# Performance work log

Hardware: AMD Instinct MI355X
Metric: run time of the kernel (lower is better)

Reference implementation:

```python
import jax, jax.numpy as jnp
import numpy as np

B, S, D, H = 2, 2048, 1024, 16
DH = D // H  # 64


def setup_inputs() -> dict:
    key = jax.random.key(0)
    k1, k2, k3 = jax.random.split(key, 3)
    return {
        "x": jax.random.normal(k1, (B, S, D), dtype=jnp.float32),
        "w_qkv": jax.random.normal(k2, (D, 3 * D), dtype=jnp.float32) * 0.02,
        "b_qkv": jnp.zeros((3 * D,), dtype=jnp.float32),
        "w_out": jax.random.normal(k3, (D, D), dtype=jnp.float32) * 0.02,
        "b_out": jnp.zeros((D,), dtype=jnp.float32),
    }


def reference(x, w_qkv, b_qkv, w_out, b_out):
    # fused qkv projection: [B,S,3D]
    qkv = x @ w_qkv + b_qkv
    q, k, v = qkv[..., :D], qkv[..., D:2 * D], qkv[..., 2 * D:]
    # split heads -> [B,H,S,DH]
    split = lambda t: t.reshape(B, S, H, DH).transpose(0, 2, 1, 3)
    q, k, v = split(q), split(k), split(v)
    scale = 1.0 / jnp.sqrt(jnp.asarray(DH, dtype=x.dtype))
    scores = jnp.einsum("bhqd,bhkd->bhqk", q, k) * scale  # [B,H,S,S]
    attn = jax.nn.softmax(scores, axis=-1)
    out = jnp.einsum("bhqk,bhkd->bhqd", attn, v)  # [B,H,S,DH]
    out = out.transpose(0, 2, 1, 3).reshape(B, S, D)
    return out @ w_out + b_out
```

## Files before the change

kernel.cpp:

```cpp
#include <hip/hip_runtime.h>
#include <cstdint>

#define B_ 2
#define S_ 2048
#define D_ 1024
#define H_ 16
#define DH_ 64

typedef short bf16x8 __attribute__((ext_vector_type(8)));
typedef float f32x4 __attribute__((ext_vector_type(4)));

__device__ inline unsigned short f2bf(float f) {
  unsigned int u = __float_as_uint(f);
  u += 0x7fffu + ((u >> 16) & 1u);
  return (unsigned short)(u >> 16);
}

__device__ inline float bf2f(unsigned short h) {
  return __uint_as_float(((unsigned int)h) << 16);
}

__device__ inline float fexp2(float x) { return __builtin_amdgcn_exp2f(x); }

__device__ inline int swz(int row, int bytecol) {
  return row * 128 + (bytecol ^ ((row & 7) << 4));
}

#define GLL(gp, lp)                                                            \
  __builtin_amdgcn_global_load_lds(                                            \
      (const __attribute__((address_space(1))) unsigned int*)(gp),             \
      (__attribute__((address_space(3))) unsigned int*)(lp), 16, 0, 0)

__global__ __launch_bounds__(256) void k_prep(const float* __restrict__ x,
                                              unsigned short* __restrict__ xb,
                                              const float* __restrict__ w_qkv,
                                              unsigned short* __restrict__ wqT,
                                              const float* __restrict__ w_out,
                                              unsigned short* __restrict__ woT) {
  __shared__ float tile[32][33];
  const int bid = blockIdx.x;
  const int t = threadIdx.x;
  if (bid < 4096) {
    int i = bid * 256 + t;
    float4 v = reinterpret_cast<const float4*>(x)[i];
    ushort4 o;
    o.x = f2bf(v.x); o.y = f2bf(v.y); o.z = f2bf(v.z); o.w = f2bf(v.w);
    reinterpret_cast<ushort4*>(xb)[i] = o;
    return;
  }
  const float* in;
  unsigned short* out;
  int R, C, bx, by;
  if (bid < 7168) {
    int id = bid - 4096;
    bx = id % 96; by = id / 96;
    in = w_qkv; out = wqT; R = 1024; C = 3072;
  } else {
    int id = bid - 7168;
    bx = id & 31; by = id >> 5;
    in = w_out; out = woT; R = 1024; C = 1024;
  }
  int ct = bx * 32, rt = by * 32;
  int tx = t & 31, ty = t >> 5;
#pragma unroll
  for (int i = 0; i < 32; i += 8)
    tile[ty + i][tx] = in[(size_t)(rt + ty + i) * C + ct + tx];
  __syncthreads();
#pragma unroll
  for (int i = 0; i < 32; i += 8)
    out[(size_t)(ct + ty + i) * R + rt + tx] = f2bf(tile[tx][ty + i]);
}

template <int BM, int BN, typename OutT>
__global__ __launch_bounds__(256) void k_gemm(const unsigned short* __restrict__ A,
                                              const unsigned short* __restrict__ BT,
                                              const float* __restrict__ bias,
                                              OutT* __restrict__ C,
                                              unsigned short* __restrict__ VTout,
                                              int M, int N, int K) {
  constexpr int MT = BM / 32, NT = BN / 32;
  __shared__ unsigned short As[BM * 64];
  __shared__ unsigned short Bs[BN * 64];
  const int t = threadIdx.x;
  const int lane = t & 63;
  const int wave = t >> 6;
  const int wm = wave >> 1, wn = wave & 1;
  const int ln15 = lane & 15, lg = lane >> 4;
  const int nwg = gridDim.x * gridDim.y;
  const int flat = blockIdx.y * gridDim.x + blockIdx.x;
  const int cpx = nwg >> 3;
  const int sid = (flat & 7) * cpx + (flat >> 3);
  const int row0 = (sid % gridDim.x) * BM, col0 = (sid / gridDim.x) * BN;
  f32x4 acc[MT][NT];
#pragma unroll
  for (int i = 0; i < MT; ++i)
#pragma unroll
    for (int j = 0; j < NT; ++j)
      acc[i][j] = (f32x4){0.f, 0.f, 0.f, 0.f};

  for (int k0 = 0; k0 < K; k0 += 64) {
    __syncthreads();
#pragma unroll
    for (int i = 0; i < BM / 32; ++i) {
      int chunk = i * 256 + t;
      int r = chunk >> 3;
      int cb = (chunk & 7) * 16;
      GLL((const char*)(A + (size_t)(row0 + r) * K + k0) + cb, (char*)As + chunk * 16);
    }
#pragma unroll
    for (int i = 0; i < BN / 32; ++i) {
      int chunk = i * 256 + t;
      int r = chunk >> 3;
      int cb = (chunk & 7) * 16;
      GLL((const char*)(BT + (size_t)(col0 + r) * K + k0) + cb, (char*)Bs + chunk * 16);
    }
    __syncthreads();
#pragma unroll
    for (int ks = 0; ks < 2; ++ks) {
      bf16x8 af[MT], bf[NT];
#pragma unroll
      for (int mt = 0; mt < MT; ++mt)
        af[mt] = *(const bf16x8*)&As[(wm * (BM / 2) + mt * 16 + ln15) * 64 + ks * 32 + lg * 8];
#pragma unroll
      for (int nt = 0; nt < NT; ++nt)
        bf[nt] = *(const bf16x8*)&Bs[(wn * (BN / 2) + nt * 16 + ln15) * 64 + ks * 32 + lg * 8];
#pragma unroll
      for (int mt = 0; mt < MT; ++mt)
#pragma unroll
        for (int nt = 0; nt < NT; ++nt)
          acc[mt][nt] = __builtin_amdgcn_mfma_f32_16x16x32_bf16(af[mt], bf[nt], acc[mt][nt], 0, 0, 0);
    }
  }
#pragma unroll
  for (int mt = 0; mt < MT; ++mt) {
#pragma unroll
    for (int nt = 0; nt < NT; ++nt) {
      int col = col0 + wn * (BN / 2) + nt * 16 + ln15;
      float bv = bias[col];
      if (VTout != nullptr && col >= 2048) {
        int hd = col - 2048;
        int row = row0 + wm * (BM / 2) + mt * 16 + lg * 4;
        int bb = row >> 11, ss = row & 2047;
        ushort4 o;
        o.x = f2bf(acc[mt][nt][0] + bv);
        o.y = f2bf(acc[mt][nt][1] + bv);
        o.z = f2bf(acc[mt][nt][2] + bv);
        o.w = f2bf(acc[mt][nt][3] + bv);
        *(ushort4*)&VTout[(((size_t)(bb * 16 + (hd >> 6)) * 64) + (hd & 63)) * 2048 + ss] = o;
      } else {
#pragma unroll
        for (int r = 0; r < 4; ++r) {
          int row = row0 + wm * (BM / 2) + mt * 16 + lg * 4 + r;
          float v = acc[mt][nt][r] + bv;
          if constexpr (sizeof(OutT) == 2)
            C[(size_t)row * N + col] = f2bf(v);
          else
            C[(size_t)row * N + col] = v;
        }
      }
    }
  }
}

__global__ __launch_bounds__(512) void k_attn(const unsigned short* __restrict__ qkv,
                                              const unsigned short* __restrict__ VT,
                                              unsigned short* __restrict__ O) {
  __shared__ unsigned short Ks[2][64 * 64];
  __shared__ unsigned short Vs[2][64 * 64];
  __shared__ unsigned short Ps[8][16 * 64];

  const int bid = blockIdx.x;
  const int xcd = bid & 7, idx = bid >> 3;
  const int bh = xcd + (idx >> 4) * 8;
  const int qblk = idx & 15;
  const int b = bh >> 4, h = bh & 15;
  const int t = threadIdx.x, wave = t >> 6, lane = t & 63;
  const int ln15 = lane & 15, lg = lane >> 4;
  const unsigned short* Qb = qkv + (size_t)b * S_ * 3072 + h * 64;
  const unsigned short* Kb = Qb + 1024;
  const unsigned short* Vb = VT + (size_t)bh * 64 * 2048;
  const int q0 = qblk * 128 + wave * 16;

  const float qsc = 0.125f * 1.4426950408889634f;
  bf16x8 qf[2];
#pragma unroll
  for (int ks = 0; ks < 2; ++ks) {
    bf16x8 raw = *(const bf16x8*)&Qb[(size_t)(q0 + ln15) * 3072 + ks * 32 + lg * 8];
#pragma unroll
    for (int j = 0; j < 8; ++j)
      qf[ks][j] = (short)f2bf(bf2f((unsigned short)raw[j]) * qsc);
  }

  const int srow = t >> 3;
  const int scol = (t & 7) ^ (srow & 7);
  const unsigned short* kPtr0 = Kb + (size_t)srow * 3072 + scol * 8;
  const unsigned short* vPtr0 = Vb + (size_t)srow * 2048 + scol * 8;
  char* ldsK0 = (char*)&Ks[0][0] + t * 16;
  char* ldsV0 = (char*)&Vs[0][0] + t * 16;

  auto stage = [&](int bi, int kv) {
    GLL(kPtr0 + (size_t)kv * 3072, ldsK0 + bi * 8192);
    GLL(vPtr0 + kv, ldsV0 + bi * 8192);
  };

  f32x4 acc[4];
#pragma unroll
  for (int dt = 0; dt < 4; ++dt)
    acc[dt] = (f32x4){0.f, 0.f, 0.f, 0.f};
  float m0 = -1e30f, l0 = 0.f;
  unsigned short* Pw = Ps[wave];

  stage(0, 0);
  __syncthreads();
  int buf = 0;

  for (int kv = 0; kv < S_; kv += 64) {
    if (kv + 64 < S_) stage(buf ^ 1, kv + 64);

    f32x4 st[4];
#pragma unroll
    for (int kg = 0; kg < 4; ++kg)
      st[kg] = (f32x4){0.f, 0.f, 0.f, 0.f};
    __builtin_amdgcn_s_setprio(1);
#pragma unroll
    for (int kg = 0; kg < 4; ++kg) {
      int krow = kg * 16 + ln15;
      bf16x8 kf0 = *(const bf16x8*)((const char*)&Ks[buf][0] + swz(krow, lg * 16));
      bf16x8 kf1 = *(const bf16x8*)((const char*)&Ks[buf][0] + swz(krow, 64 + lg * 16));
      st[kg] = __builtin_amdgcn_mfma_f32_16x16x32_bf16(kf0, qf[0], st[kg], 0, 0, 0);
      st[kg] = __builtin_amdgcn_mfma_f32_16x16x32_bf16(kf1, qf[1], st[kg], 0, 0, 0);
    }
    __builtin_amdgcn_s_setprio(0);

    float tm = -1e30f;
#pragma unroll
    for (int kg = 0; kg < 4; ++kg)
      tm = fmaxf(tm, fmaxf(fmaxf(st[kg][0], st[kg][1]),
                           fmaxf(st[kg][2], st[kg][3])));
    tm = fmaxf(tm, __shfl_xor(tm, 16));
    tm = fmaxf(tm, __shfl_xor(tm, 32));

    if (__any(tm > m0 + 11.0f)) {
      float n0 = fmaxf(m0, tm);
      float r0 = fexp2(m0 - n0);
      m0 = n0; l0 *= r0;
#pragma unroll
      for (int dt = 0; dt < 4; ++dt)
#pragma unroll
        for (int r = 0; r < 4; ++r)
          acc[dt][r] *= r0;
    }

    asm volatile("" ::: "memory");
    float ts = 0.f;
#pragma unroll
    for (int kg = 0; kg < 4; ++kg) {
      float p0 = fexp2(st[kg][0] - m0);
      float p1 = fexp2(st[kg][1] - m0);
      float p2 = fexp2(st[kg][2] - m0);
      float p3 = fexp2(st[kg][3] - m0);
      ts += (p0 + p1) + (p2 + p3);
      unsigned int w0, w1;
      asm("v_cvt_pk_bf16_f32 %0, %1, %2" : "=v"(w0) : "v"(p0), "v"(p1));
      asm("v_cvt_pk_bf16_f32 %0, %1, %2" : "=v"(w1) : "v"(p2), "v"(p3));
      *(uint2*)((char*)Pw + swz(ln15, kg * 32 + lg * 8)) = make_uint2(w0, w1);
    }
    ts += __shfl_xor(ts, 16);
    ts += __shfl_xor(ts, 32);
    l0 += ts;
    asm volatile("" ::: "memory");

    __builtin_amdgcn_s_setprio(1);
#pragma unroll
    for (int kc = 0; kc < 2; ++kc) {
      bf16x8 pf = *(const bf16x8*)((const char*)Pw + swz(ln15, kc * 64 + lg * 16));
#pragma unroll
      for (int dt = 0; dt < 4; ++dt) {
        bf16x8 vf = *(const bf16x8*)((const char*)&Vs[buf][0] + swz(dt * 16 + ln15, kc * 64 + lg * 16));
        acc[dt] = __builtin_amdgcn_mfma_f32_16x16x32_bf16(vf, pf, acc[dt], 0, 0, 0);
      }
    }
    __builtin_amdgcn_s_setprio(0);
    __syncthreads();
    buf ^= 1;
  }

  float inv = 1.f / l0;
  size_t qglob = q0 + ln15;
  size_t base = ((size_t)b * S_ + qglob) * D_ + h * 64 + lg * 4;
#pragma unroll
  for (int dt = 0; dt < 4; ++dt) {
    ushort4 o;
    o.x = f2bf(acc[dt][0] * inv);
    o.y = f2bf(acc[dt][1] * inv);
    o.z = f2bf(acc[dt][2] * inv);
    o.w = f2bf(acc[dt][3] * inv);
    *(ushort4*)&O[base + (size_t)dt * 16] = o;
  }
}

extern "C" void kernel_launch(void* const* d_in, const int* in_sizes, int n_in,
                              void* d_out, int out_size, void* d_ws, size_t ws_size,
                              hipStream_t stream) {
  const float* x     = (const float*)d_in[0];
  const float* w_qkv = (const float*)d_in[1];
  const float* b_qkv = (const float*)d_in[2];
  const float* w_out = (const float*)d_in[3];
  const float* b_out = (const float*)d_in[4];
  float* out = (float*)d_out;

  char* ws = (char*)d_ws;
  const size_t MiB = (size_t)1 << 20;
  unsigned short* xb   = (unsigned short*)(ws + 0 * MiB);
  unsigned short* wqT  = (unsigned short*)(ws + 8 * MiB);
  unsigned short* woT  = (unsigned short*)(ws + 14 * MiB);
  unsigned short* qkvb = (unsigned short*)(ws + 16 * MiB);
  unsigned short* VTb  = (unsigned short*)(ws + 40 * MiB);
  unsigned short* Ab   = (unsigned short*)(ws + 48 * MiB);

  k_prep<<<8192, 256, 0, stream>>>(x, xb, w_qkv, wqT, w_out, woT);
  k_gemm<128, 128, unsigned short><<<dim3(32, 24), 256, 0, stream>>>(xb, wqT, b_qkv, qkvb, VTb, 4096, 3072, 1024);
  k_attn<<<512, 512, 0, stream>>>(qkvb, VTb, Ab);
  k_gemm<128, 64, float><<<dim3(32, 16), 256, 0, stream>>>(Ab, woT, b_out, out, nullptr, 4096, 1024, 1024);
}
```

Measured before the change: 217.1 us.

## Replace QKV GEMM with 256x256 double-buffered 8-wave pipelined kernel

Adds a new GEMM kernel with 256x256 tiles, 512 threads, double-buffered swizzled LDS, and global loads staged in four pieces interleaved with MFMA quarters, using partial vmcnt waits and setprio. It replaces the QKV projection GEMM, which now runs on 192 workgroups instead of 768. The intent is to overlap global-to-LDS transfers with compute and get more operand reuse per tile. The risks are low grid occupancy on a 256-CU device (192 blocks), heavy register pressure, and fragile hand-written waitcnt logic. The V-transpose epilogue is removed from the old kernel, which now only serves the output GEMM.

```diff
diff --git a/kernel.cpp b/kernel.cpp
--- a/kernel.cpp
+++ b/kernel.cpp
@@ -71,6 +71,163 @@
     out[(size_t)(ct + ty + i) * R + rt + tx] = f2bf(tile[tx][ty + i]);
 }
 
+#define READB(p)                                                               \
+  _Pragma("unroll") for (int nt = 0; nt < 4; ++nt)                             \
+  _Pragma("unroll") for (int ks = 0; ks < 2; ++ks)                             \
+      bf[nt][ks] = *(const bf16x8*)((const char*)&Bs[cur][0] +                 \
+                   swz((p) * 64 + nt * 16 + ln15, ks * 64 + lg * 16));
+
+#define STAGEPIECE(h)                                                          \
+  _Pragma("unroll") for (int j = 0; j < 2; ++j) {                              \
+    const int rr = ((h) & 1) * 128 + srow + 64 * j;                            \
+    const int gc = scol8 ^ (rr & 7);                                           \
+    const unsigned short* gsrc =                                               \
+        (((h) < 2) ? (A + (size_t)(row0 + rr) * K)                             \
+                   : (BT + (size_t)(col0 + rr) * K)) + k0n + gc * 8;           \
+    char* ldst = (char*)(((h) < 2) ? &As[cur ^ 1][0] : &Bs[cur ^ 1][0]) +      \
+                 rr * 128 + scol8 * 16;                                        \
+    GLL(gsrc, ldst);                                                           \
+  }
+
+#define MFMAQ(p)                                                               \
+  _Pragma("unroll") for (int mt = 0; mt < 2; ++mt)                             \
+  _Pragma("unroll") for (int nt = 0; nt < 4; ++nt) {                           \
+    acc[mt][(p) * 4 + nt] = __builtin_amdgcn_mfma_f32_16x16x32_bf16(           \
+        af[mt][0], bf[nt][0], acc[mt][(p) * 4 + nt], 0, 0, 0);                 \
+    acc[mt][(p) * 4 + nt] = __builtin_amdgcn_mfma_f32_16x16x32_bf16(           \
+        af[mt][1], bf[nt][1], acc[mt][(p) * 4 + nt], 0, 0, 0);                 \
+  }
+
+template <typename OutT>
+__global__ __launch_bounds__(512, 2) void k_gemm8(const unsigned short* __restrict__ A,
+                                                  const unsigned short* __restrict__ BT,
+                                                  const float* __restrict__ bias,
+                                                  OutT* __restrict__ C,
+                                                  unsigned short* __restrict__ VTout,
+                                                  int M, int N, int K) {
+  __shared__ unsigned short As[2][256 * 64];
+  __shared__ unsigned short Bs[2][256 * 64];
+  const int t = threadIdx.x;
+  const int lane = t & 63;
+  const int w = t >> 6;
+  const int ln15 = lane & 15, lg = lane >> 4;
+  const int srow = t >> 3;
+  const int scol8 = t & 7;
+  const int nwg = gridDim.x * gridDim.y;
+  const int flat = blockIdx.y * gridDim.x + blockIdx.x;
+  const int cpx = nwg >> 3;
+  const int sid = (flat & 7) * cpx + (flat >> 3);
+  const int row0 = (sid % gridDim.x) * 256, col0 = (sid / gridDim.x) * 256;
+
+  f32x4 acc[2][16];
+#pragma unroll
+  for (int i = 0; i < 2; ++i)
+#pragma unroll
+    for (int j = 0; j < 16; ++j)
+      acc[i][j] = (f32x4){0.f, 0.f, 0.f, 0.f};
+
+  const int NTILES = K / 64;
+  {
+    const int k0n = 0;
+    const int cur = 1;
+    STAGEPIECE(0); STAGEPIECE(1); STAGEPIECE(2); STAGEPIECE(3);
+  }
+  asm volatile("s_waitcnt vmcnt(0)" ::: "memory");
+  __builtin_amdgcn_s_barrier();
+
+  int cur = 0;
+  for (int kt = 0; kt < NTILES; ++kt) {
+    const int k0n = (kt + 1) * 64;
+    const bool more = (kt + 1) < NTILES;
+    bf16x8 af[2][2];
+    {
+      bf16x8 bf[4][2];
+      READB(0);
+#pragma unroll
+      for (int mt = 0; mt < 2; ++mt)
+#pragma unroll
+        for (int ks = 0; ks < 2; ++ks)
+          af[mt][ks] = *(const bf16x8*)((const char*)&As[cur][0] +
+                       swz(w * 32 + mt * 16 + ln15, ks * 64 + lg * 16));
+      if (more) { STAGEPIECE(0); }
+      __builtin_amdgcn_s_barrier();
+      __builtin_amdgcn_s_setprio(1);
+      MFMAQ(0);
+      __builtin_amdgcn_s_setprio(0);
+      __builtin_amdgcn_s_barrier();
+    }
+    {
+      bf16x8 bf[4][2];
+      READB(1);
+      if (more) {
+        STAGEPIECE(1);
+        asm volatile("s_waitcnt vmcnt(4)" ::: "memory");
+      } else {
+        asm volatile("s_waitcnt vmcnt(0)" ::: "memory");
+      }
+      __builtin_amdgcn_s_barrier();
+      __builtin_amdgcn_s_setprio(1);
+      MFMAQ(1);
+      __builtin_amdgcn_s_setprio(0);
+      __builtin_amdgcn_s_barrier();
+    }
+    {
+      bf16x8 bf[4][2];
+      READB(2);
+      if (more) { STAGEPIECE(2); }
+      __builtin_amdgcn_s_barrier();
+      __builtin_amdgcn_s_setprio(1);
+      MFMAQ(2);
+      __builtin_amdgcn_s_setprio(0);
+      __builtin_amdgcn_s_barrier();
+    }
+    {
+      bf16x8 bf[4][2];
+      READB(3);
+      if (more) {
+        STAGEPIECE(3);
+        asm volatile("s_waitcnt vmcnt(2)" ::: "memory");
+      }
+      __builtin_amdgcn_s_barrier();
+      __builtin_amdgcn_s_setprio(1);
+      MFMAQ(3);
+      __builtin_amdgcn_s_setprio(0);
+      __builtin_amdgcn_s_barrier();
+    }
+    cur ^= 1;
+  }
+
+#pragma unroll
+  for (int mt = 0; mt < 2; ++mt) {
+#pragma unroll
+    for (int nt = 0; nt < 16; ++nt) {
+      int col = col0 + nt * 16 + ln15;
+      float bv = bias[col];
+      if (VTout != nullptr && col >= 2048) {
+        int hd = col - 2048;
+        int row = row0 + w * 32 + mt * 16 + lg * 4;
+        int bb = row >> 11, ss = row & 2047;
+        ushort4 o;
+        o.x = f2bf(acc[mt][nt][0] + bv);
+        o.y = f2bf(acc[mt][nt][1] + bv);
+        o.z = f2bf(acc[mt][nt][2] + bv);
+        o.w = f2bf(acc[mt][nt][3] + bv);
+        *(ushort4*)&VTout[(((size_t)(bb * 16 + (hd >> 6)) * 64) + (hd & 63)) * 2048 + ss] = o;
+      } else {
+#pragma unroll
+        for (int r = 0; r < 4; ++r) {
+          int row = row0 + w * 32 + mt * 16 + lg * 4 + r;
+          float v = acc[mt][nt][r] + bv;
+          if constexpr (sizeof(OutT) == 2)
+            C[(size_t)row * N + col] = f2bf(v);
+          else
+            C[(size_t)row * N + col] = v;
+        }
+      }
+    }
+  }
+}
+
 template <int BM, int BN, typename OutT>
 __global__ __launch_bounds__(256) void k_gemm(const unsigned short* __restrict__ A,
                                               const unsigned short* __restrict__ BT,
@@ -79,8 +236,8 @@
                                               unsigned short* __restrict__ VTout,
                                               int M, int N, int K) {
   constexpr int MT = BM / 32, NT = BN / 32;
-  __shared__ unsigned short As[BM * 64];
-  __shared__ unsigned short Bs[BN * 64];
+  __shared__ unsigned short As2[BM * 64];
+  __shared__ unsigned short Bs2[BN * 64];
   const int t = threadIdx.x;
   const int lane = t & 63;
   const int wave = t >> 6;
@@ -105,14 +262,14 @@
       int chunk = i * 256 + t;
       int r = chunk >> 3;
       int cb = (chunk & 7) * 16;
-      GLL((const char*)(A + (size_t)(row0 + r) * K + k0) + cb, (char*)As + chunk * 16);
+      GLL((const char*)(A + (size_t)(row0 + r) * K + k0) + cb, (char*)As2 + chunk * 16);
     }
 #pragma unroll
     for (int i = 0; i < BN / 32; ++i) {
       int chunk = i * 256 + t;
       int r = chunk >> 3;
       int cb = (chunk & 7) * 16;
-      GLL((const char*)(BT + (size_t)(col0 + r) * K + k0) + cb, (char*)Bs + chunk * 16);
+      GLL((const char*)(BT + (size_t)(col0 + r) * K + k0) + cb, (char*)Bs2 + chunk * 16);
     }
     __syncthreads();
 #pragma unroll
@@ -120,10 +277,10 @@
       bf16x8 af[MT], bf[NT];
 #pragma unroll
       for (int mt = 0; mt < MT; ++mt)
-        af[mt] = *(const bf16x8*)&As[(wm * (BM / 2) + mt * 16 + ln15) * 64 + ks * 32 + lg * 8];
+        af[mt] = *(const bf16x8*)&As2[(wm * (BM / 2) + mt * 16 + ln15) * 64 + ks * 32 + lg * 8];
 #pragma unroll
       for (int nt = 0; nt < NT; ++nt)
-        bf[nt] = *(const bf16x8*)&Bs[(wn * (BN / 2) + nt * 16 + ln15) * 64 + ks * 32 + lg * 8];
+        bf[nt] = *(const bf16x8*)&Bs2[(wn * (BN / 2) + nt * 16 + ln15) * 64 + ks * 32 + lg * 8];
 #pragma unroll
       for (int mt = 0; mt < MT; ++mt)
 #pragma unroll
@@ -137,26 +294,14 @@
     for (int nt = 0; nt < NT; ++nt) {
       int col = col0 + wn * (BN / 2) + nt * 16 + ln15;
       float bv = bias[col];
-      if (VTout != nullptr && col >= 2048) {
-        int hd = col - 2048;
-        int row = row0 + wm * (BM / 2) + mt * 16 + lg * 4;
-        int bb = row >> 11, ss = row & 2047;
-        ushort4 o;
-        o.x = f2bf(acc[mt][nt][0] + bv);
-        o.y = f2bf(acc[mt][nt][1] + bv);
-        o.z = f2bf(acc[mt][nt][2] + bv);
-        o.w = f2bf(acc[mt][nt][3] + bv);
-        *(ushort4*)&VTout[(((size_t)(bb * 16 + (hd >> 6)) * 64) + (hd & 63)) * 2048 + ss] = o;
-      } else {
-#pragma unroll
-        for (int r = 0; r < 4; ++r) {
-          int row = row0 + wm * (BM / 2) + mt * 16 + lg * 4 + r;
-          float v = acc[mt][nt][r] + bv;
-          if constexpr (sizeof(OutT) == 2)
-            C[(size_t)row * N + col] = f2bf(v);
-          else
-            C[(size_t)row * N + col] = v;
-        }
+#pragma unroll
+      for (int r = 0; r < 4; ++r) {
+        int row = row0 + wm * (BM / 2) + mt * 16 + lg * 4 + r;
+        float v = acc[mt][nt][r] + bv;
+        if constexpr (sizeof(OutT) == 2)
+          C[(size_t)row * N + col] = f2bf(v);
+        else
+          C[(size_t)row * N + col] = v;
       }
     }
   }
@@ -319,7 +464,7 @@
   unsigned short* Ab   = (unsigned short*)(ws + 48 * MiB);
 
   k_prep<<<8192, 256, 0, stream>>>(x, xb, w_qkv, wqT, w_out, woT);
-  k_gemm<128, 128, unsigned short><<<dim3(32, 24), 256, 0, stream>>>(xb, wqT, b_qkv, qkvb, VTb, 4096, 3072, 1024);
+  k_gemm8<unsigned short><<<dim3(16, 12), 512, 0, stream>>>(xb, wqT, b_qkv, qkvb, VTb, 4096, 3072, 1024);
   k_attn<<<512, 512, 0, stream>>>(qkvb, VTb, Ab);
   k_gemm<128, 64, float><<<dim3(32, 16), 256, 0, stream>>>(Ab, woT, b_out, out, nullptr, 4096, 1024, 1024);
 }
```

Result: faster. 200.9 us (-7.5%).
